# Optimization experiments

Hardware: AMD Instinct MI355X
Metric: run time of the kernel (lower is better)

The kernel has to match this reference:

```python
import jax, jax.numpy as jnp
import numpy as np

N = 10000       # nodes
E = 160000      # edges (avg degree 16)
WIDTH = 256
SCALE = 2
HID = WIDTH * SCALE   # 512
HEAD_DIM = 64
EW = WIDTH // 2       # edge embed width = 128
BOND = (5, 6, 2, 17)
RES = 1.0


def _lin(key, fan_in, fan_out):
    kw, kb = jax.random.split(key)
    s = 1.0 / np.sqrt(fan_in)
    W = jax.random.uniform(kw, (fan_in, fan_out), minval=-s, maxval=s, dtype=jnp.float32)
    b = jax.random.uniform(kb, (fan_out,), minval=-s, maxval=s, dtype=jnp.float32)
    return W, b


def setup_inputs() -> dict:
    key = jax.random.key(0)
    ks = jax.random.split(key, 24)
    inp = {}
    inp['x'] = jax.random.normal(ks[0], (N, WIDTH), dtype=jnp.float32)
    inp['edge_index'] = jax.random.randint(ks[1], (2, E), 0, N, dtype=jnp.int32)
    inp['edge_attr'] = jax.random.randint(ks[2], (E, 4), 0, 3, dtype=jnp.int32)
    inp['edge_embed'] = jax.random.normal(ks[3], (E, EW), dtype=jnp.float32)
    # EmbedBlock tables: size[i]+1 rows; tables 1..3 have padding_idx=0 (row 0 zeroed)
    inp['emb0'] = jax.random.normal(ks[4], (BOND[0] + 1, EW), dtype=jnp.float32)
    for i, k in zip((1, 2, 3), (ks[5], ks[6], ks[7])):
        t = jax.random.normal(k, (BOND[i] + 1, EW), dtype=jnp.float32)
        inp[f'emb{i}'] = t.at[0].set(0.0)
    # learned log-scales (torch inits to zeros; use small values so paths are non-trivial)
    inp['init0_e'] = 0.1 * jax.random.normal(ks[8], (4,), dtype=jnp.float32)
    inp['init0'] = 0.1 * jax.random.normal(ks[9], (4,), dtype=jnp.float32)  # hop*2+2 = 4
    inp['W_pre'], inp['b_pre'] = _lin(ks[10], WIDTH, WIDTH)
    inp['W_msg0'], inp['b_msg0'] = _lin(ks[11], WIDTH, HID)
    inp['W_q'], inp['b_q'] = _lin(ks[12], WIDTH, HID)
    inp['W_k'], inp['b_k'] = _lin(ks[13], WIDTH, HID)
    inp['W_v'], inp['b_v'] = _lin(ks[14], WIDTH, HID)
    inp['W_r0'], inp['b_r0'] = _lin(ks[15], EW, HID)
    inp['W_r1'], inp['b_r1'] = _lin(ks[16], EW, HID)
    inp['W_r2'], inp['b_r2'] = _lin(ks[17], EW, HID)
    inp['W_post'], inp['b_post'] = _lin(ks[18], HID, WIDTH)
    return inp


def _ln(h):
    m = h.mean(-1, keepdims=True)
    v = ((h - m) ** 2).mean(-1, keepdims=True)
    return (h - m) / jnp.sqrt(v + 1e-5)


def _gelu(h):
    return jax.nn.gelu(h, approximate=False)  # torch nn.GELU default (erf)


def reference(x, edge_index, edge_attr, edge_embed,
              emb0, emb1, emb2, emb3, init0_e, init0,
              W_pre, b_pre, W_msg0, b_msg0, W_q, b_q, W_k, b_k, W_v, b_v,
              W_r0, b_r0, W_r1, b_r1, W_r2, b_r2, W_post, b_post):
    # pre: Linear + LayerNorm(no affine)
    xx = _ln(x @ W_pre + b_pre)                                  # [N, W]
    # EmbedBlock(bond_size): weighted sum of 4 embeddings, then average with x_ema
    xw = jnp.exp(init0_e) / jnp.sqrt(jnp.sum(jnp.exp(init0_e)))
    ee = (emb0[edge_attr[:, 0]] * xw[0] + emb1[edge_attr[:, 1]] * xw[1]
          + emb2[edge_attr[:, 2]] * xw[2] + emb3[edge_attr[:, 3]] * xw[3])  # [E, EW]
    ee = (ee + edge_embed) / 2
    # message: gather endpoints (source_to_target: row0=j source, row1=i target)
    src, dst = edge_index[0], edge_index[1]
    x_i = xx[dst]                                                # [E, W]
    x_j = xx[src]                                                # [E, W]
    s_e = jnp.exp(init0[-2])
    s_v = jnp.exp(init0[-1])
    x_q = x_i @ W_q + b_q + (ee @ W_r0 + b_r0) * s_e             # [E, HID]
    x_k = x_j @ W_k + b_k + (ee @ W_r1 + b_r1) * s_e
    x_v = _gelu(x_j @ W_v + b_v + (ee @ W_r2 + b_r2) * s_v)
    # inline per-edge multi-head dot-product attention
    att = jnp.sum((x_q * x_k).reshape(E, -1, HEAD_DIM), axis=-1, keepdims=True) / np.sqrt(HEAD_DIM)
    att = jnp.exp(att * init0[0] + init0[1])                     # [E, H, 1]
    msg = (x_v.reshape(E, -1, HEAD_DIM) * att).reshape(E, HID)
    # scatter-add aggregation at targets
    agg = jax.ops.segment_sum(msg, dst, num_segments=N)          # [N, HID]
    xx2 = _gelu(xx @ W_msg0 + b_msg0) + agg
    out = x + (xx2 @ W_post + b_post) * RES                      # [N, W]
    return out
```

## Files before the change

kernel.cpp:

```cpp
#include <hip/hip_runtime.h>
#include <hip/hip_bf16.h>
#include <math.h>

#define NN   10000
#define EE   160000
#define WID  256
#define HIDD 512
#define EWID 128

typedef __attribute__((ext_vector_type(8))) short bf16x8;
typedef __attribute__((ext_vector_type(4))) float f32x4;

__device__ __forceinline__ float geluf(float x) {
    return 0.5f * x * (1.0f + erff(x * 0.70710678118654752f));
}

__device__ __forceinline__ unsigned short f2bf(float f) {
    unsigned int u = __float_as_uint(f);
    u += 0x7fffu + ((u >> 16) & 1u);
    return (unsigned short)(u >> 16);
}

__device__ __forceinline__ float bfup(unsigned int u, int hi) {
    return hi ? __uint_as_float(u & 0xffff0000u) : __uint_as_float(u << 16);
}

__global__ __launch_bounds__(256) void k_cvt(const float* __restrict__ W0,
                                             const float* __restrict__ W1,
                                             const float* __restrict__ W2,
                                             unsigned short* __restrict__ out) {
    int tid = blockIdx.x * 256 + threadIdx.x;
    int p = tid >> 16;
    int rem = tid & 65535;
    int n = rem >> 7, k = rem & 127;
    const float* W = p == 0 ? W0 : p == 1 ? W1 : W2;
    out[tid] = f2bf(W[k * HIDD + n]);
}

__global__ __launch_bounds__(256) void k_cvtn(const float* __restrict__ W0,
                                              const float* __restrict__ W1,
                                              const float* __restrict__ W2,
                                              const float* __restrict__ W3,
                                              unsigned short* __restrict__ out) {
    int tid = blockIdx.x * 256 + threadIdx.x;
    int sel = tid >> 17;
    int rem = tid & 131071;
    int n = rem >> 8, k = rem & 255;
    const float* W = sel == 0 ? W0 : sel == 1 ? W1 : sel == 2 ? W2 : W3;
    out[tid] = f2bf(W[k * HIDD + n]);
}

__global__ __launch_bounds__(256) void k_cvt2(const float* __restrict__ Wpre,
                                              const float* __restrict__ Wpost,
                                              unsigned short* __restrict__ WpreT,
                                              unsigned short* __restrict__ WpostT) {
    int tid = blockIdx.x * 256 + threadIdx.x;
    if (tid < 65536) {
        int n = tid >> 8, k = tid & 255;
        WpreT[tid] = f2bf(Wpre[k * WID + n]);
    } else {
        int rem = tid - 65536;
        int n = rem >> 9, k = rem & 511;
        WpostT[rem] = f2bf(Wpost[k * WID + n]);
    }
}

__global__ __launch_bounds__(256, 4) void k_pre(const float* __restrict__ x,
                                                const unsigned short* __restrict__ WpreT,
                                                const float* __restrict__ bp,
                                                unsigned short* __restrict__ xxb) {
    __shared__ __align__(16) float ot[16 * 260];
    int t = threadIdx.x;
    int lane = t & 63, w = t >> 6;
    int l15 = lane & 15, quad = lane >> 4;
    int r0 = blockIdx.x * 16;
    bf16x8 af[8];
    #pragma unroll
    for (int kb = 0; kb < 8; ++kb) {
        int k0 = kb * 32 + quad * 8;
        float a8[8];
        *(float4*)&a8[0] = *(const float4*)&x[(r0 + l15) * WID + k0];
        *(float4*)&a8[4] = *(const float4*)&x[(r0 + l15) * WID + k0 + 4];
        bf16x8 p;
        #pragma unroll
        for (int j = 0; j < 8; ++j) p[j] = (short)f2bf(a8[j]);
        af[kb] = p;
    }
    #pragma unroll
    for (int tb = 0; tb < 4; ++tb) {
        int c = w * 64 + tb * 16 + l15;
        float bias = bp[c];
        f32x4 acc = {bias, bias, bias, bias};
        #pragma unroll
        for (int kb = 0; kb < 8; ++kb) {
            bf16x8 bfr = *(const bf16x8*)&WpreT[c * WID + kb * 32 + quad * 8];
            acc = __builtin_amdgcn_mfma_f32_16x16x32_bf16(af[kb], bfr, acc, 0, 0, 0);
        }
        #pragma unroll
        for (int r = 0; r < 4; ++r)
            ot[(quad * 4 + r) * 260 + c] = acc[r];
    }
    __syncthreads();
    #pragma unroll
    for (int rr = 0; rr < 4; ++rr) {
        int row = w * 4 + rr;
        float s = 0.f, s2 = 0.f;
        #pragma unroll
        for (int k2 = 0; k2 < 4; ++k2) {
            float v = ot[row * 260 + lane + 64 * k2];
            s += v; s2 += v * v;
        }
        #pragma unroll
        for (int off = 32; off >= 1; off >>= 1) {
            s  += __shfl_xor(s,  off, 64);
            s2 += __shfl_xor(s2, off, 64);
        }
        float m = s * (1.f / WID);
        float rstd = rsqrtf(s2 * (1.f / WID) - m * m + 1e-5f);
        #pragma unroll
        for (int k2 = 0; k2 < 4; ++k2) {
            int c = lane + 64 * k2;
            xxb[(r0 + row) * WID + c] = f2bf((ot[row * 260 + c] - m) * rstd);
        }
    }
}

__global__ __launch_bounds__(256, 4) void k_qkvm(
    const unsigned short* __restrict__ xxb,
    const unsigned short* __restrict__ WTn,
    const float* __restrict__ bq, const float* __restrict__ bk,
    const float* __restrict__ bv, const float* __restrict__ bm,
    unsigned short* __restrict__ XQp, unsigned short* __restrict__ XKp,
    unsigned short* __restrict__ XVp, float* __restrict__ AG) {
    int t = threadIdx.x;
    int r0 = blockIdx.x * 16;
    int sel = blockIdx.y;
    const float* bsel = sel == 0 ? bq : sel == 1 ? bk : sel == 2 ? bv : bm;
    const unsigned short* Wp = WTn + sel * (HIDD * WID);
    unsigned short* outp = sel == 0 ? XQp : sel == 1 ? XKp : XVp;
    int lane = t & 63, w = t >> 6;
    int l15 = lane & 15, quad = lane >> 4;
    bf16x8 af[8];
    #pragma unroll
    for (int kb = 0; kb < 8; ++kb)
        af[kb] = *(const bf16x8*)&xxb[(r0 + l15) * WID + kb * 32 + quad * 8];
    #pragma unroll
    for (int tb = 0; tb < 8; ++tb) {
        int c = w * 128 + tb * 16;
        float bias = bsel[c + l15];
        f32x4 acc = {bias, bias, bias, bias};
        #pragma unroll
        for (int kb = 0; kb < 8; ++kb) {
            bf16x8 bfr = *(const bf16x8*)&Wp[(c + l15) * WID + kb * 32 + quad * 8];
            acc = __builtin_amdgcn_mfma_f32_16x16x32_bf16(af[kb], bfr, acc, 0, 0, 0);
        }
        if (sel < 3) {
            int base = ((w * 64 + (tb >> 1) * 16 + l15) << 1) + (tb & 1);
            #pragma unroll
            for (int r = 0; r < 4; ++r) {
                int node = r0 + quad * 4 + r;
                outp[node * 512 + base] = f2bf(acc[r]);
            }
        } else {
            #pragma unroll
            for (int r = 0; r < 4; ++r) {
                int node = r0 + quad * 4 + r;
                AG[node * HIDD + c + l15] = geluf(acc[r]);
            }
        }
    }
}

__global__ __launch_bounds__(256, 4) void k_edge(
    const int* __restrict__ eidx, const int* __restrict__ eattr,
    const float* __restrict__ eemb,
    const float* __restrict__ emb0, const float* __restrict__ emb1,
    const float* __restrict__ emb2, const float* __restrict__ emb3,
    const float* __restrict__ i0e, const float* __restrict__ i0,
    const unsigned int* __restrict__ XQp, const unsigned int* __restrict__ XKp,
    const unsigned int* __restrict__ XVp,
    const unsigned short* __restrict__ WrT,
    const float* __restrict__ br0, const float* __restrict__ br1,
    const float* __restrict__ br2,
    float* __restrict__ agg) {
    __shared__ __align__(16) unsigned short Bs[128 * 136];
    int t = threadIdx.x;
    int lane = t & 63, w = t >> 6;
    int l15 = lane & 15, quad = lane >> 4;
    int cg = blockIdx.x;
    int e0 = blockIdx.y * 64 + w * 16;

    float ev0 = __expf(i0e[0]), ev1 = __expf(i0e[1]),
          ev2 = __expf(i0e[2]), ev3 = __expf(i0e[3]);
    float rsum = rsqrtf(ev0 + ev1 + ev2 + ev3);
    float xw0 = ev0 * rsum, xw1 = ev1 * rsum, xw2 = ev2 * rsum, xw3 = ev3 * rsum;
    float a_sc = i0[0], a_bi = i0[1];
    float s_e = expf(i0[2]), s_v = expf(i0[3]);
    float c_sc = 0.125f * a_sc;

    int me = e0 + l15;
    int4 at = *(const int4*)&eattr[me * 4];
    bf16x8 af[4];
    #pragma unroll
    for (int kb = 0; kb < 4; ++kb) {
        int k0 = kb * 32 + quad * 8;
        float t0[8], t1[8], t2[8], t3[8], te[8];
        *(float4*)&t0[0] = *(const float4*)&emb0[at.x * EWID + k0];
        *(float4*)&t0[4] = *(const float4*)&emb0[at.x * EWID + k0 + 4];
        *(float4*)&t1[0] = *(const float4*)&emb1[at.y * EWID + k0];
        *(float4*)&t1[4] = *(const float4*)&emb1[at.y * EWID + k0 + 4];
        *(float4*)&t2[0] = *(const float4*)&emb2[at.z * EWID + k0];
        *(float4*)&t2[4] = *(const float4*)&emb2[at.z * EWID + k0 + 4];
        *(float4*)&t3[0] = *(const float4*)&emb3[at.w * EWID + k0];
        *(float4*)&t3[4] = *(const float4*)&emb3[at.w * EWID + k0 + 4];
        *(float4*)&te[0] = *(const float4*)&eemb[me * EWID + k0];
        *(float4*)&te[4] = *(const float4*)&eemb[me * EWID + k0 + 4];
        bf16x8 p;
        #pragma unroll
        for (int j = 0; j < 8; ++j)
            p[j] = (short)f2bf(0.5f * (xw0 * t0[j] + xw1 * t1[j] + xw2 * t2[j]
                                       + xw3 * t3[j] + te[j]));
        af[kb] = p;
    }

    int ndp[4], nsp[4], nda[4];
    #pragma unroll
    for (int r = 0; r < 4; ++r) {
        int en = e0 + quad * 4 + r;
        int sn = eidx[en], dn = eidx[EE + en];
        ndp[r] = dn * 256 + cg * 64 + l15;
        nsp[r] = sn * 256 + cg * 64 + l15;
        nda[r] = dn * HIDD + cg * 128 + l15;
    }

    unsigned int pq[4][4], pk[4][4];
    #pragma unroll
    for (int a = 0; a < 4; ++a)
        #pragma unroll
        for (int r = 0; r < 4; ++r) {
            pq[a][r] = XQp[ndp[r] + a * 16];
            pk[a][r] = XKp[nsp[r] + a * 16];
        }

    int sc = t >> 1, skh = (t & 1) * 64;
    const uint4* ssrc = (const uint4*)&WrT[(cg * 128 + sc) * 128 + skh];
    uint4* sdst = (uint4*)&Bs[sc * 136 + skh];

    #pragma unroll
    for (int i = 0; i < 8; ++i) sdst[i] = ssrc[i];
    __syncthreads();
    float q[8][4];
    #pragma unroll
    for (int tb = 0; tb < 8; ++tb) {
        int cl = tb * 16 + l15;
        float bias = br0[cg * 128 + cl];
        f32x4 acc = {bias, bias, bias, bias};
        #pragma unroll
        for (int kb = 0; kb < 4; ++kb) {
            bf16x8 bfr = *(const bf16x8*)&Bs[cl * 136 + kb * 32 + quad * 8];
            acc = __builtin_amdgcn_mfma_f32_16x16x32_bf16(af[kb], bfr, acc, 0, 0, 0);
        }
        #pragma unroll
        for (int r = 0; r < 4; ++r)
            q[tb][r] = bfup(pq[tb >> 1][r], tb & 1) + s_e * acc[r];
    }
    unsigned int pv[4][4];
    #pragma unroll
    for (int a = 0; a < 4; ++a)
        #pragma unroll
        for (int r = 0; r < 4; ++r) pv[a][r] = XVp[nsp[r] + a * 16];
    __syncthreads();

    #pragma unroll
    for (int i = 0; i < 8; ++i) sdst[i] = ssrc[8192 + i];
    __syncthreads();
    float d0[4] = {0.f, 0.f, 0.f, 0.f}, d1[4] = {0.f, 0.f, 0.f, 0.f};
    #pragma unroll
    for (int tb = 0; tb < 8; ++tb) {
        int cl = tb * 16 + l15;
        float bias = br1[cg * 128 + cl];
        f32x4 acc = {bias, bias, bias, bias};
        #pragma unroll
        for (int kb = 0; kb < 4; ++kb) {
            bf16x8 bfr = *(const bf16x8*)&Bs[cl * 136 + kb * 32 + quad * 8];
            acc = __builtin_amdgcn_mfma_f32_16x16x32_bf16(af[kb], bfr, acc, 0, 0, 0);
        }
        #pragma unroll
        for (int r = 0; r < 4; ++r) {
            float kv = bfup(pk[tb >> 1][r], tb & 1) + s_e * acc[r];
            float pp = q[tb][r] * kv;
            if (tb < 4) d0[r] += pp; else d1[r] += pp;
        }
    }
    float att0[4], att1[4];
    #pragma unroll
    for (int off = 8; off >= 1; off >>= 1) {
        #pragma unroll
        for (int r = 0; r < 4; ++r) {
            d0[r] += __shfl_xor(d0[r], off, 64);
            d1[r] += __shfl_xor(d1[r], off, 64);
        }
    }
    #pragma unroll
    for (int r = 0; r < 4; ++r) {
        att0[r] = expf(d0[r] * c_sc + a_bi);
        att1[r] = expf(d1[r] * c_sc + a_bi);
    }
    __syncthreads();

    #pragma unroll
    for (int i = 0; i < 8; ++i) sdst[i] = ssrc[16384 + i];
    __syncthreads();
    #pragma unroll
    for (int tb = 0; tb < 8; ++tb) {
        int cl = tb * 16 + l15;
        float bias = br2[cg * 128 + cl];
        f32x4 acc = {bias, bias, bias, bias};
        #pragma unroll
        for (int kb = 0; kb < 4; ++kb) {
            bf16x8 bfr = *(const bf16x8*)&Bs[cl * 136 + kb * 32 + quad * 8];
            acc = __builtin_amdgcn_mfma_f32_16x16x32_bf16(af[kb], bfr, acc, 0, 0, 0);
        }
        #pragma unroll
        for (int r = 0; r < 4; ++r) {
            float v = geluf(bfup(pv[tb >> 1][r], tb & 1) + s_v * acc[r]);
            float m = v * (tb < 4 ? att0[r] : att1[r]);
            atomicAdd(&agg[nda[r] + tb * 16], m);
        }
    }
}

__global__ __launch_bounds__(256, 4) void k_post(const float* __restrict__ x,
    const float* __restrict__ agg,
    const unsigned short* __restrict__ WpT,
    const float* __restrict__ bp,
    float* __restrict__ out) {
    int t = threadIdx.x;
    int lane = t & 63, w = t >> 6;
    int l15 = lane & 15, quad = lane >> 4;
    int r0 = blockIdx.x * 16;
    bf16x8 af[16];
    #pragma unroll
    for (int kb = 0; kb < 16; ++kb) {
        int k0 = kb * 32 + quad * 8;
        float a8[8];
        *(float4*)&a8[0] = *(const float4*)&agg[(r0 + l15) * HIDD + k0];
        *(float4*)&a8[4] = *(const float4*)&agg[(r0 + l15) * HIDD + k0 + 4];
        bf16x8 p;
        #pragma unroll
        for (int j = 0; j < 8; ++j) p[j] = (short)f2bf(a8[j]);
        af[kb] = p;
    }
    #pragma unroll
    for (int tb = 0; tb < 4; ++tb) {
        int c = w * 64 + tb * 16 + l15;
        float bias = bp[c];
        f32x4 acc = {bias, bias, bias, bias};
        #pragma unroll
        for (int kb = 0; kb < 16; ++kb) {
            bf16x8 bfr = *(const bf16x8*)&WpT[c * HIDD + kb * 32 + quad * 8];
            acc = __builtin_amdgcn_mfma_f32_16x16x32_bf16(af[kb], bfr, acc, 0, 0, 0);
        }
        #pragma unroll
        for (int r = 0; r < 4; ++r) {
            int row = r0 + quad * 4 + r;
            out[row * WID + c] = x[row * WID + c] + acc[r];
        }
    }
}

extern "C" void kernel_launch(void* const* d_in, const int* in_sizes, int n_in,
                              void* d_out, int out_size, void* d_ws, size_t ws_size,
                              hipStream_t stream) {
    const float* x     = (const float*)d_in[0];
    const int*   eidx  = (const int*)  d_in[1];
    const int*   eattr = (const int*)  d_in[2];
    const float* eemb  = (const float*)d_in[3];
    const float* emb0  = (const float*)d_in[4];
    const float* emb1  = (const float*)d_in[5];
    const float* emb2  = (const float*)d_in[6];
    const float* emb3  = (const float*)d_in[7];
    const float* i0e   = (const float*)d_in[8];
    const float* i0    = (const float*)d_in[9];
    const float* Wpre  = (const float*)d_in[10];
    const float* bpre  = (const float*)d_in[11];
    const float* Wm    = (const float*)d_in[12];
    const float* bm    = (const float*)d_in[13];
    const float* Wq    = (const float*)d_in[14];
    const float* bq    = (const float*)d_in[15];
    const float* Wk    = (const float*)d_in[16];
    const float* bk    = (const float*)d_in[17];
    const float* Wv    = (const float*)d_in[18];
    const float* bv    = (const float*)d_in[19];
    const float* Wr0   = (const float*)d_in[20];
    const float* br0   = (const float*)d_in[21];
    const float* Wr1   = (const float*)d_in[22];
    const float* br1   = (const float*)d_in[23];
    const float* Wr2   = (const float*)d_in[24];
    const float* br2   = (const float*)d_in[25];
    const float* Wpost = (const float*)d_in[26];
    const float* bpost = (const float*)d_in[27];

    float* ws  = (float*)d_ws;
    float* agg = ws;
    unsigned short* xxb    = (unsigned short*)(ws + 5120000);
    unsigned short* XQp    = (unsigned short*)(ws + 6400000);
    unsigned short* XKp    = (unsigned short*)(ws + 8960000);
    unsigned short* XVp    = (unsigned short*)(ws + 11520000);
    unsigned short* WrT    = (unsigned short*)(ws + 14080000);
    unsigned short* WTn    = (unsigned short*)(ws + 14178304);
    unsigned short* WpreT  = (unsigned short*)(ws + 14440448);
    unsigned short* WpostT = (unsigned short*)(ws + 14473216);

    k_cvt<<<768, 256, 0, stream>>>(Wr0, Wr1, Wr2, WrT);
    k_cvtn<<<2048, 256, 0, stream>>>(Wq, Wk, Wv, Wm, WTn);
    k_cvt2<<<768, 256, 0, stream>>>(Wpre, Wpost, WpreT, WpostT);
    k_pre<<<625, 256, 0, stream>>>(x, WpreT, bpre, xxb);
    k_qkvm<<<dim3(625, 4), 256, 0, stream>>>(xxb, WTn, bq, bk, bv, bm,
                                             XQp, XKp, XVp, agg);
    k_edge<<<dim3(4, 2500), 256, 0, stream>>>(eidx, eattr, eemb,
                                              emb0, emb1, emb2, emb3,
                                              i0e, i0,
                                              (const unsigned int*)XQp,
                                              (const unsigned int*)XKp,
                                              (const unsigned int*)XVp,
                                              WrT, br0, br1, br2, agg);
    k_post<<<625, 256, 0, stream>>>(x, agg, WpostT, bpost, (float*)d_out);
}
```

Baseline: 758.5 us.

## Precompute edge embeddings once, retile qkvm to 32 rows, relayout LDS weights

```diff
diff --git a/kernel.cpp b/kernel.cpp
--- a/kernel.cpp
+++ b/kernel.cpp
@@ -65,6 +65,42 @@
     }
 }
 
+__global__ __launch_bounds__(256) void k_ee(
+    const int* __restrict__ eattr, const float* __restrict__ eemb,
+    const float* __restrict__ emb0, const float* __restrict__ emb1,
+    const float* __restrict__ emb2, const float* __restrict__ emb3,
+    const float* __restrict__ i0e,
+    unsigned short* __restrict__ eeF) {
+    int c = blockIdx.x * 256 + threadIdx.x;
+    int lane6 = c & 63;
+    int kb = (c >> 6) & 3;
+    int tile = c >> 8;
+    int edge = tile * 16 + (lane6 & 15);
+    int k0 = kb * 32 + (lane6 >> 4) * 8;
+    float ev0 = __expf(i0e[0]), ev1 = __expf(i0e[1]),
+          ev2 = __expf(i0e[2]), ev3 = __expf(i0e[3]);
+    float rsum = rsqrtf(ev0 + ev1 + ev2 + ev3);
+    float xw0 = ev0 * rsum, xw1 = ev1 * rsum, xw2 = ev2 * rsum, xw3 = ev3 * rsum;
+    int4 at = *(const int4*)&eattr[edge * 4];
+    float t0[8], t1[8], t2[8], t3[8], te[8];
+    *(float4*)&t0[0] = *(const float4*)&emb0[at.x * EWID + k0];
+    *(float4*)&t0[4] = *(const float4*)&emb0[at.x * EWID + k0 + 4];
+    *(float4*)&t1[0] = *(const float4*)&emb1[at.y * EWID + k0];
+    *(float4*)&t1[4] = *(const float4*)&emb1[at.y * EWID + k0 + 4];
+    *(float4*)&t2[0] = *(const float4*)&emb2[at.z * EWID + k0];
+    *(float4*)&t2[4] = *(const float4*)&emb2[at.z * EWID + k0 + 4];
+    *(float4*)&t3[0] = *(const float4*)&emb3[at.w * EWID + k0];
+    *(float4*)&t3[4] = *(const float4*)&emb3[at.w * EWID + k0 + 4];
+    *(float4*)&te[0] = *(const float4*)&eemb[edge * EWID + k0];
+    *(float4*)&te[4] = *(const float4*)&eemb[edge * EWID + k0 + 4];
+    bf16x8 p;
+    #pragma unroll
+    for (int j = 0; j < 8; ++j)
+        p[j] = (short)f2bf(0.5f * (xw0 * t0[j] + xw1 * t1[j] + xw2 * t2[j]
+                                   + xw3 * t3[j] + te[j]));
+    *(bf16x8*)&eeF[c * 8] = p;
+}
+
 __global__ __launch_bounds__(256, 4) void k_pre(const float* __restrict__ x,
                                                 const unsigned short* __restrict__ WpreT,
                                                 const float* __restrict__ bp,
@@ -133,95 +169,80 @@
     unsigned short* __restrict__ XQp, unsigned short* __restrict__ XKp,
     unsigned short* __restrict__ XVp, float* __restrict__ AG) {
     int t = threadIdx.x;
-    int r0 = blockIdx.x * 16;
+    int r0 = blockIdx.x * 32;
     int sel = blockIdx.y;
     const float* bsel = sel == 0 ? bq : sel == 1 ? bk : sel == 2 ? bv : bm;
     const unsigned short* Wp = WTn + sel * (HIDD * WID);
     unsigned short* outp = sel == 0 ? XQp : sel == 1 ? XKp : XVp;
     int lane = t & 63, w = t >> 6;
     int l15 = lane & 15, quad = lane >> 4;
-    bf16x8 af[8];
-    #pragma unroll
-    for (int kb = 0; kb < 8; ++kb)
-        af[kb] = *(const bf16x8*)&xxb[(r0 + l15) * WID + kb * 32 + quad * 8];
+    int rA = min(r0 + l15, NN - 1);
+    int rB = min(r0 + 16 + l15, NN - 1);
+    bf16x8 af0[8], af1[8];
+    #pragma unroll
+    for (int kb = 0; kb < 8; ++kb) {
+        af0[kb] = *(const bf16x8*)&xxb[rA * WID + kb * 32 + quad * 8];
+        af1[kb] = *(const bf16x8*)&xxb[rB * WID + kb * 32 + quad * 8];
+    }
     #pragma unroll
     for (int tb = 0; tb < 8; ++tb) {
         int c = w * 128 + tb * 16;
         float bias = bsel[c + l15];
-        f32x4 acc = {bias, bias, bias, bias};
+        f32x4 acc0 = {bias, bias, bias, bias};
+        f32x4 acc1 = {bias, bias, bias, bias};
         #pragma unroll
         for (int kb = 0; kb < 8; ++kb) {
             bf16x8 bfr = *(const bf16x8*)&Wp[(c + l15) * WID + kb * 32 + quad * 8];
-            acc = __builtin_amdgcn_mfma_f32_16x16x32_bf16(af[kb], bfr, acc, 0, 0, 0);
+            acc0 = __builtin_amdgcn_mfma_f32_16x16x32_bf16(af0[kb], bfr, acc0, 0, 0, 0);
+            acc1 = __builtin_amdgcn_mfma_f32_16x16x32_bf16(af1[kb], bfr, acc1, 0, 0, 0);
         }
         if (sel < 3) {
             int base = ((w * 64 + (tb >> 1) * 16 + l15) << 1) + (tb & 1);
             #pragma unroll
             for (int r = 0; r < 4; ++r) {
-                int node = r0 + quad * 4 + r;
-                outp[node * 512 + base] = f2bf(acc[r]);
+                int n0 = r0 + quad * 4 + r;
+                int n1 = n0 + 16;
+                if (n0 < NN) outp[n0 * 512 + base] = f2bf(acc0[r]);
+                if (n1 < NN) outp[n1 * 512 + base] = f2bf(acc1[r]);
             }
         } else {
             #pragma unroll
             for (int r = 0; r < 4; ++r) {
-                int node = r0 + quad * 4 + r;
-                AG[node * HIDD + c + l15] = geluf(acc[r]);
+                int n0 = r0 + quad * 4 + r;
+                int n1 = n0 + 16;
+                if (n0 < NN) AG[n0 * HIDD + c + l15] = geluf(acc0[r]);
+                if (n1 < NN) AG[n1 * HIDD + c + l15] = geluf(acc1[r]);
             }
         }
     }
 }
 
 __global__ __launch_bounds__(256, 4) void k_edge(
-    const int* __restrict__ eidx, const int* __restrict__ eattr,
-    const float* __restrict__ eemb,
-    const float* __restrict__ emb0, const float* __restrict__ emb1,
-    const float* __restrict__ emb2, const float* __restrict__ emb3,
-    const float* __restrict__ i0e, const float* __restrict__ i0,
+    const int* __restrict__ eidx,
+    const unsigned short* __restrict__ eeF,
+    const float* __restrict__ i0,
     const unsigned int* __restrict__ XQp, const unsigned int* __restrict__ XKp,
     const unsigned int* __restrict__ XVp,
     const unsigned short* __restrict__ WrT,
     const float* __restrict__ br0, const float* __restrict__ br1,
     const float* __restrict__ br2,
     float* __restrict__ agg) {
-    __shared__ __align__(16) unsigned short Bs[128 * 136];
+    __shared__ __align__(16) unsigned short Bs[2048 * 8];
     int t = threadIdx.x;
     int lane = t & 63, w = t >> 6;
     int l15 = lane & 15, quad = lane >> 4;
     int cg = blockIdx.x;
-    int e0 = blockIdx.y * 64 + w * 16;
-
-    float ev0 = __expf(i0e[0]), ev1 = __expf(i0e[1]),
-          ev2 = __expf(i0e[2]), ev3 = __expf(i0e[3]);
-    float rsum = rsqrtf(ev0 + ev1 + ev2 + ev3);
-    float xw0 = ev0 * rsum, xw1 = ev1 * rsum, xw2 = ev2 * rsum, xw3 = ev3 * rsum;
+    int tile = blockIdx.y * 4 + w;
+    int e0 = tile * 16;
+
     float a_sc = i0[0], a_bi = i0[1];
     float s_e = expf(i0[2]), s_v = expf(i0[3]);
     float c_sc = 0.125f * a_sc;
 
-    int me = e0 + l15;
-    int4 at = *(const int4*)&eattr[me * 4];
     bf16x8 af[4];
     #pragma unroll
-    for (int kb = 0; kb < 4; ++kb) {
-        int k0 = kb * 32 + quad * 8;
-        float t0[8], t1[8], t2[8], t3[8], te[8];
-        *(float4*)&t0[0] = *(const float4*)&emb0[at.x * EWID + k0];
-        *(float4*)&t0[4] = *(const float4*)&emb0[at.x * EWID + k0 + 4];
-        *(float4*)&t1[0] = *(const float4*)&emb1[at.y * EWID + k0];
-        *(float4*)&t1[4] = *(const float4*)&emb1[at.y * EWID + k0 + 4];
-        *(float4*)&t2[0] = *(const float4*)&emb2[at.z * EWID + k0];
-        *(float4*)&t2[4] = *(const float4*)&emb2[at.z * EWID + k0 + 4];
-        *(float4*)&t3[0] = *(const float4*)&emb3[at.w * EWID + k0];
-        *(float4*)&t3[4] = *(const float4*)&emb3[at.w * EWID + k0 + 4];
-        *(float4*)&te[0] = *(const float4*)&eemb[me * EWID + k0];
-        *(float4*)&te[4] = *(const float4*)&eemb[me * EWID + k0 + 4];
-        bf16x8 p;
-        #pragma unroll
-        for (int j = 0; j < 8; ++j)
-            p[j] = (short)f2bf(0.5f * (xw0 * t0[j] + xw1 * t1[j] + xw2 * t2[j]
-                                       + xw3 * t3[j] + te[j]));
-        af[kb] = p;
-    }
+    for (int kb = 0; kb < 4; ++kb)
+        af[kb] = *(const bf16x8*)&eeF[((tile * 4 + kb) * 64 + lane) * 8];
 
     int ndp[4], nsp[4], nda[4];
     #pragma unroll
@@ -242,22 +263,20 @@
             pk[a][r] = XKp[nsp[r] + a * 16];
         }
 
-    int sc = t >> 1, skh = (t & 1) * 64;
-    const uint4* ssrc = (const uint4*)&WrT[(cg * 128 + sc) * 128 + skh];
-    uint4* sdst = (uint4*)&Bs[sc * 136 + skh];
-
-    #pragma unroll
-    for (int i = 0; i < 8; ++i) sdst[i] = ssrc[i];
+    const bf16x8* ssrc0 = (const bf16x8*)&WrT[(cg * 128 + l15) * 128 + w * 32 + quad * 8];
+    bf16x8* sdst0 = (bf16x8*)&Bs[(w * 64 + lane) * 8];
+
+    #pragma unroll
+    for (int i = 0; i < 8; ++i) sdst0[i * 256] = ssrc0[i * 16 * 16];
     __syncthreads();
     float q[8][4];
     #pragma unroll
     for (int tb = 0; tb < 8; ++tb) {
-        int cl = tb * 16 + l15;
-        float bias = br0[cg * 128 + cl];
+        float bias = br0[cg * 128 + tb * 16 + l15];
         f32x4 acc = {bias, bias, bias, bias};
         #pragma unroll
         for (int kb = 0; kb < 4; ++kb) {
-            bf16x8 bfr = *(const bf16x8*)&Bs[cl * 136 + kb * 32 + quad * 8];
+            bf16x8 bfr = *(const bf16x8*)&Bs[(tb * 256 + kb * 64 + lane) * 8];
             acc = __builtin_amdgcn_mfma_f32_16x16x32_bf16(af[kb], bfr, acc, 0, 0, 0);
         }
         #pragma unroll
@@ -272,17 +291,16 @@
     __syncthreads();
 
     #pragma unroll
-    for (int i = 0; i < 8; ++i) sdst[i] = ssrc[8192 + i];
+    for (int i = 0; i < 8; ++i) sdst0[i * 256] = ssrc0[8192 + i * 256];
     __syncthreads();
     float d0[4] = {0.f, 0.f, 0.f, 0.f}, d1[4] = {0.f, 0.f, 0.f, 0.f};
     #pragma unroll
     for (int tb = 0; tb < 8; ++tb) {
-        int cl = tb * 16 + l15;
-        float bias = br1[cg * 128 + cl];
+        float bias = br1[cg * 128 + tb * 16 + l15];
         f32x4 acc = {bias, bias, bias, bias};
         #pragma unroll
         for (int kb = 0; kb < 4; ++kb) {
-            bf16x8 bfr = *(const bf16x8*)&Bs[cl * 136 + kb * 32 + quad * 8];
+            bf16x8 bfr = *(const bf16x8*)&Bs[(tb * 256 + kb * 64 + lane) * 8];
             acc = __builtin_amdgcn_mfma_f32_16x16x32_bf16(af[kb], bfr, acc, 0, 0, 0);
         }
         #pragma unroll
@@ -309,16 +327,15 @@
     __syncthreads();
 
     #pragma unroll
-    for (int i = 0; i < 8; ++i) sdst[i] = ssrc[16384 + i];
+    for (int i = 0; i < 8; ++i) sdst0[i * 256] = ssrc0[16384 + i * 256];
     __syncthreads();
     #pragma unroll
     for (int tb = 0; tb < 8; ++tb) {
-        int cl = tb * 16 + l15;
-        float bias = br2[cg * 128 + cl];
+        float bias = br2[cg * 128 + tb * 16 + l15];
         f32x4 acc = {bias, bias, bias, bias};
         #pragma unroll
         for (int kb = 0; kb < 4; ++kb) {
-            bf16x8 bfr = *(const bf16x8*)&Bs[cl * 136 + kb * 32 + quad * 8];
+            bf16x8 bfr = *(const bf16x8*)&Bs[(tb * 256 + kb * 64 + lane) * 8];
             acc = __builtin_amdgcn_mfma_f32_16x16x32_bf16(af[kb], bfr, acc, 0, 0, 0);
         }
         #pragma unroll
@@ -411,16 +428,16 @@
     unsigned short* WTn    = (unsigned short*)(ws + 14178304);
     unsigned short* WpreT  = (unsigned short*)(ws + 14440448);
     unsigned short* WpostT = (unsigned short*)(ws + 14473216);
+    unsigned short* eeF    = (unsigned short*)(ws + 14538752);
 
     k_cvt<<<768, 256, 0, stream>>>(Wr0, Wr1, Wr2, WrT);
     k_cvtn<<<2048, 256, 0, stream>>>(Wq, Wk, Wv, Wm, WTn);
     k_cvt2<<<768, 256, 0, stream>>>(Wpre, Wpost, WpreT, WpostT);
+    k_ee<<<10000, 256, 0, stream>>>(eattr, eemb, emb0, emb1, emb2, emb3, i0e, eeF);
     k_pre<<<625, 256, 0, stream>>>(x, WpreT, bpre, xxb);
-    k_qkvm<<<dim3(625, 4), 256, 0, stream>>>(xxb, WTn, bq, bk, bv, bm,
+    k_qkvm<<<dim3(313, 4), 256, 0, stream>>>(xxb, WTn, bq, bk, bv, bm,
                                              XQp, XKp, XVp, agg);
-    k_edge<<<dim3(4, 2500), 256, 0, stream>>>(eidx, eattr, eemb,
-                                              emb0, emb1, emb2, emb3,
-                                              i0e, i0,
+    k_edge<<<dim3(4, 2500), 256, 0, stream>>>(eidx, eeF, i0,
                                               (const unsigned int*)XQp,
                                               (const unsigned int*)XKp,
                                               (const unsigned int*)XVp,
```

Result: faster. 694.0 us (-8.5%).
